# Kernel optimization log

Hardware: AMD Instinct MI355X
Metric: run time of the kernel (lower is better)

Reference implementation:

```python
import jax, jax.numpy as jnp
import numpy as np
import math

B, S, H, NH = 2, 2048, 2048, 16
HD = H // NH
LAYER_NUMBER = 5
NORM_FACTOR = math.sqrt(HD) * LAYER_NUMBER  # sqrt(head_dim) * coeff
BETA = 1.0 / LAYER_NUMBER
SCALE = float(LAYER_NUMBER)  # ScaledSoftmax scale = coeff
MASK_VALUE = -10000.0


def setup_inputs() -> dict:
    key = jax.random.key(0)
    ks = jax.random.split(key, 6)
    inv_sqrt_h = 1.0 / math.sqrt(H)
    return {
        "hidden_states": jax.random.normal(ks[0], (B, S, H), jnp.float32),
        "alibi": jax.random.normal(ks[1], (NH, 1, S), jnp.float32) * 0.1,
        "w_qkv": jax.random.normal(ks[2], (3 * H, H), jnp.float32) * inv_sqrt_h,
        "b_qkv": jax.random.normal(ks[3], (3 * H,), jnp.float32) * 0.02,
        "w_dense": jax.random.normal(ks[4], (H, H), jnp.float32) * inv_sqrt_h,
        "b_dense": jax.random.normal(ks[5], (H,), jnp.float32) * 0.02,
        "attention_mask": jnp.ones((B, S), jnp.int32),
    }


def reference(hidden_states, alibi, w_qkv, b_qkv, w_dense, b_dense, attention_mask):
    b, s, h = hidden_states.shape
    # QKV projection: [b, s, 3h] -> [b, s, nh, 3*hd] -> split
    mixed = hidden_states @ w_qkv.T + b_qkv
    mixed = mixed.reshape(b, s, NH, 3 * HD)
    q, k, v = jnp.split(mixed, 3, axis=-1)  # each [b, s, nh, hd]

    # Faithful Megatron-style memory reinterpretation (row-major reshape),
    # exactly matching torch's .contiguous().view(s, b*nh, hd).
    q2 = jnp.swapaxes(q.reshape(s, b * NH, HD), 0, 1)  # [b*nh, q_len, hd]
    k2 = jnp.swapaxes(k.reshape(s, b * NH, HD), 0, 1)  # [b*nh, k_len, hd]
    v2 = jnp.swapaxes(v.reshape(s, b * NH, HD), 0, 1)  # [b*nh, k_len, hd]

    # baddbmm: alibi*beta + (q @ k^T)/norm_factor
    alibi_b = jnp.tile(alibi, (b, 1, 1))[: b * NH, :, :s]  # [b*nh, 1, k_len]
    scores = alibi_b * BETA + jnp.einsum("bqd,bkd->bqk", q2, k2) * (1.0 / NORM_FACTOR)
    scores = scores.reshape(b, NH, s, s)

    # ScaledSoftmax: scale then fused causal+padding mask fill, then softmax
    scores = scores * SCALE
    pad_bool = (1 - attention_mask).astype(bool)  # True where padded
    causal = jnp.tril(jnp.ones((s, s), dtype=bool))
    bad = pad_bool[:, None, :, None] | (~causal)[None, None, :, :]  # [b,1,s,s]
    scores = jnp.where(bad, MASK_VALUE, scores)
    probs = jax.nn.softmax(scores, axis=-1)  # [b, nh, s, s]

    # context = probs @ V with the same faithful reshapes
    probs_r = probs.reshape(b * NH, s, s)
    context = jnp.einsum("bqk,bkd->bqd", probs_r, v2)  # [b*nh, q_len, hd]
    context = context.reshape(b, NH, s, HD)
    context = jnp.transpose(context, (2, 0, 1, 3)).reshape(s, b, h)  # [s, b, h]

    out = context @ w_dense.T + b_dense  # [s, b, h]
    return jnp.swapaxes(out, 0, 1)  # [b, s, h]
```

## Files before the change

### kernel.cpp

```cpp
#include <hip/hip_runtime.h>

typedef unsigned short u16;
typedef __bf16  bf16x8 __attribute__((ext_vector_type(8)));
typedef float   f32x4  __attribute__((ext_vector_type(4)));
typedef u16     u16x8  __attribute__((ext_vector_type(8)));
typedef u16     u16x4  __attribute__((ext_vector_type(4)));

#define QSCALE 0.12751744545f

__device__ __forceinline__ u16 f2b(float f) {
    unsigned u = __float_as_uint(f);
    unsigned r = u + 0x7FFFu + ((u >> 16) & 1u);
    return (u16)(r >> 16);
}
__device__ __forceinline__ float b2f(u16 b) {
    return __uint_as_float(((unsigned)b) << 16);
}
__device__ __forceinline__ void async16(const u16* g, u16* l) {
    __builtin_amdgcn_global_load_lds(
        (__attribute__((address_space(1))) void*)(u16*)g,
        (__attribute__((address_space(3))) void*)l, 16, 0, 0);
}

__global__ void cvt_f32_bf16(const float* __restrict__ in, u16* __restrict__ out, int n4) {
    int i = blockIdx.x * blockDim.x + threadIdx.x;
    if (i >= n4) return;
    float4 f = ((const float4*)in)[i];
    u16x4 o;
    o[0] = f2b(f.x); o[1] = f2b(f.y); o[2] = f2b(f.z); o[3] = f2b(f.w);
    *(u16x4*)(out + (size_t)i * 4) = o;
}

__global__ void cvt_wqkv(const float* __restrict__ in, u16* __restrict__ out, int n4) {
    int i = blockIdx.x * blockDim.x + threadIdx.x;
    if (i >= n4) return;
    int row = i >> 9;
    float s = ((row % 384) < 128) ? QSCALE : 1.0f;
    float4 f = ((const float4*)in)[i];
    u16x4 o;
    o[0] = f2b(f.x * s); o[1] = f2b(f.y * s); o[2] = f2b(f.z * s); o[3] = f2b(f.w * s);
    *(u16x4*)(out + (size_t)i * 4) = o;
}

__global__ __launch_bounds__(256) void gemm_bt(
    const u16* __restrict__ A, const u16* __restrict__ B,
    const float* __restrict__ bias, void* __restrict__ C,
    u16* __restrict__ qb, u16* __restrict__ kb, u16* __restrict__ vb,
    int M, int N, int K, int mode)
{
    __shared__ u16 smem[16384];
    u16* As = smem;
    u16* Bs = smem + 8192;

    int tid = threadIdx.x, wave = tid >> 6, lane = tid & 63;
    int lg = lane >> 4, lm = lane & 15;
    int wm = (wave & 1) * 64, wn = (wave >> 1) * 64;

    const u16* Ab = A + (size_t)(blockIdx.y * 128) * K;
    const u16* Bb = B + (size_t)(blockIdx.x * 128) * K;

    f32x4 acc[4][4];
    for (int i = 0; i < 4; i++)
        for (int j = 0; j < 4; j++)
            acc[i][j] = (f32x4){0.f, 0.f, 0.f, 0.f};

    int srow = (lane >> 2), skq = (lane & 3) * 8;

    for (int k0 = 0; k0 < K; k0 += 64) {
        __syncthreads();
        for (int cc = wave; cc < 16; cc += 4) {
            int p = cc >> 3, c = cc & 7;
            int row = c * 16 + srow;
            size_t off = (size_t)row * K + k0 + p * 32 + skq;
            async16(Ab + off, &As[p * 4096 + c * 512]);
            async16(Bb + off, &Bs[p * 4096 + c * 512]);
        }
        __syncthreads();

        for (int p = 0; p < 2; p++) {
            bf16x8 af[4], bf[4];
            for (int i = 0; i < 4; i++) af[i] = *(const bf16x8*)&As[p * 4096 + (wm + i * 16 + lm) * 32 + lg * 8];
            for (int j = 0; j < 4; j++) bf[j] = *(const bf16x8*)&Bs[p * 4096 + (wn + j * 16 + lm) * 32 + lg * 8];
            for (int i = 0; i < 4; i++)
                for (int j = 0; j < 4; j++)
                    acc[i][j] = __builtin_amdgcn_mfma_f32_16x16x32_bf16(af[i], bf[j], acc[i][j], 0, 0, 0);
        }
    }

    if (mode == 1) {
        for (int j = 0; j < 4; j++) {
            int col = blockIdx.x * 128 + wn + j * 16 + lm;
            float bv = bias[col];
            for (int i = 0; i < 4; i++) {
                int row0 = blockIdx.y * 128 + wm + i * 16 + lg * 4;
                for (int r = 0; r < 4; r++) {
                    int row = row0 + r;
                    int orow = ((row & 1) << 11) + (row >> 1);
                    ((float*)C)[(size_t)orow * N + col] = acc[i][j][r] + bv;
                }
            }
        }
        return;
    }

    int ct = blockIdx.x;
    int nh = ct / 3, part = ct - nh * 3;
    float bscale = (part == 0) ? QSCALE : 1.0f;
    int rbase = blockIdx.y * 128;
    int b = rbase >> 11;
    int s0 = rbase & 2047;

    if (part < 2) {
        u16* dst0 = part ? kb : qb;
        for (int j = 0; j < 4; j++) {
            int hd = wn + j * 16 + lm;
            float bv = bias[ct * 128 + hd] * bscale;
            for (int i = 0; i < 4; i++) {
                for (int r = 0; r < 4; r++) {
                    int rl = wm + i * 16 + lg * 4 + r;
                    int s = s0 + rl;
                    int bn = (s & 1) * 16 + nh;
                    int pos = (b << 10) + (s >> 1);
                    dst0[((size_t)(bn * 2048 + pos)) * 128 + hd] = f2b(acc[i][j][r] + bv);
                }
            }
        }
    } else {
        u16 (*arr)[64][128] = (u16(*)[64][128])smem;
        __syncthreads();
        for (int j = 0; j < 4; j++) {
            int hd = wn + j * 16 + lm;
            float bv = bias[ct * 128 + hd];
            for (int i = 0; i < 4; i++) {
                for (int r = 0; r < 4; r++) {
                    int rl = wm + i * 16 + lg * 4 + r;
                    arr[rl & 1][rl >> 1][hd] = f2b(acc[i][j][r] + bv);
                }
            }
        }
        __syncthreads();
        int hd = tid & 127, par = tid >> 7;
        int bn = par * 16 + nh;
        int pos0 = (b << 10) + (s0 >> 1);
        u16* dst = vb + ((size_t)(bn * 128 + hd)) * 2048 + pos0;
        for (int c = 0; c < 8; c++) {
            u16x8 w;
            for (int e = 0; e < 8; e++) w[e] = arr[par][c * 8 + e][hd];
            *(u16x8*)(dst + c * 8) = w;
        }
    }
}

__global__ __launch_bounds__(256) void attn(
    const u16* __restrict__ qb, const u16* __restrict__ kb,
    const u16* __restrict__ vb, const float* __restrict__ alibi,
    u16* __restrict__ ctx)
{
    __shared__ u16 Ks[64 * 136];
    __shared__ u16 Vt[128 * 88];
    __shared__ u16 Ps[4][16 * 72];

    int bn = blockIdx.y;
    int tid = threadIdx.x, wave = tid >> 6, lane = tid & 63;
    int lg = lane >> 4, lm = lane & 15;

    const float* al = alibi + (bn & 15) * 2048;

    int krow = tid >> 2, kq = (tid & 3) * 32;
    int vhd  = tid >> 1, vh2 = (tid & 1) * 32;
    const u16* ksrc0 = kb + (size_t)(bn * 2048 + krow) * 128 + kq;
    const u16* vsrc0 = vb + (size_t)(bn * 128 + vhd) * 2048 + vh2;

    u16* ps = &Ps[wave][0];
    bf16x8 ones;
    {
        u16x8 t;
        for (int j = 0; j < 8; j++) t[j] = 0x3F80;
        ones = *(bf16x8*)&t;
    }

    for (int pass = 0; pass < 2; pass++) {
        int qt = pass ? (31 - blockIdx.x) : blockIdx.x;
        int q0 = qt * 64;

        bf16x8 qf[4];
        {
            const u16* qp = qb + ((size_t)bn * 2048 + q0 + wave * 16 + lm) * 128 + lg * 8;
            for (int kc = 0; kc < 4; kc++) qf[kc] = *(const bf16x8*)(qp + kc * 32);
        }

        f32x4 o[9];
        for (int i = 0; i < 9; i++) o[i] = (f32x4){0.f, 0.f, 0.f, 0.f};

        u16x8 kreg[4], vreg[4];
        for (int i = 0; i < 4; i++) kreg[i] = *(const u16x8*)(ksrc0 + i * 8);
        for (int i = 0; i < 4; i++) vreg[i] = *(const u16x8*)(vsrc0 + i * 8);

        for (int kt = 0; kt <= qt; kt++) {
            int k0 = kt * 64;
            __syncthreads();
            {
                u16* d1 = &Ks[krow * 136 + kq];
                for (int i = 0; i < 4; i++) *(u16x8*)(d1 + i * 8) = kreg[i];
                u16* d2 = &Vt[vhd * 88 + vh2];
                for (int i = 0; i < 4; i++) *(u16x8*)(d2 + i * 8) = vreg[i];
            }
            __syncthreads();

            if (kt < qt) {
                const u16* s1 = ksrc0 + (size_t)(kt + 1) * 64 * 128;
                const u16* s2 = vsrc0 + (kt + 1) * 64;
                for (int i = 0; i < 4; i++) kreg[i] = *(const u16x8*)(s1 + i * 8);
                for (int i = 0; i < 4; i++) vreg[i] = *(const u16x8*)(s2 + i * 8);
            }

            f32x4 sc[4];
            for (int tc = 0; tc < 4; tc++) {
                const u16* kr = &Ks[(tc * 16 + lm) * 136 + lg * 8];
                f32x4 a = (f32x4){0.f, 0.f, 0.f, 0.f};
                for (int kc = 0; kc < 4; kc++)
                    a = __builtin_amdgcn_mfma_f32_16x16x32_bf16(qf[kc], *(const bf16x8*)(kr + kc * 32), a, 0, 0, 0);
                sc[tc] = a;
            }

            bool diag = (kt == qt);
            for (int tc = 0; tc < 4; tc++) {
                int kg = k0 + tc * 16 + lm;
                float av = (al[kg] - 8.0f) * 1.4426950408889634f;
                for (int r = 0; r < 4; r++) {
                    float v = sc[tc][r] + av;
                    if (diag && kg > q0 + wave * 16 + lg * 4 + r) v = -3e38f;
                    ps[(lg * 4 + r) * 72 + tc * 16 + lm] = f2b(__builtin_amdgcn_exp2f(v));
                }
            }

            for (int kc = 0; kc < 2; kc++) {
                bf16x8 pf = *(const bf16x8*)&ps[lm * 72 + kc * 32 + lg * 8];
                for (int i = 0; i < 8; i++) {
                    bf16x8 vf = *(const bf16x8*)&Vt[(i * 16 + lm) * 88 + kc * 32 + lg * 8];
                    o[i] = __builtin_amdgcn_mfma_f32_16x16x32_bf16(pf, vf, o[i], 0, 0, 0);
                }
                o[8] = __builtin_amdgcn_mfma_f32_16x16x32_bf16(pf, ones, o[8], 0, 0, 0);
            }
        }

        for (int r = 0; r < 4; r++) {
            float inv = 1.0f / o[8][r];
            int qg = q0 + wave * 16 + lg * 4 + r;
            int row = qg * 2 + (bn >> 4);
            u16* crow = ctx + (size_t)row * 2048 + (bn & 15) * 128 + lm;
            for (int i = 0; i < 8; i++)
                crow[i * 16] = f2b(o[i][r] * inv);
        }
    }
}

extern "C" void kernel_launch(void* const* d_in, const int* in_sizes, int n_in,
                              void* d_out, int out_size, void* d_ws, size_t ws_size,
                              hipStream_t stream)
{
    const float* hs    = (const float*)d_in[0];
    const float* alibi = (const float*)d_in[1];
    const float* wqkv  = (const float*)d_in[2];
    const float* bqkv  = (const float*)d_in[3];
    const float* wd    = (const float*)d_in[4];
    const float* bd    = (const float*)d_in[5];
    float* out = (float*)d_out;

    char* ws = (char*)d_ws;
    u16* wqkv_b = (u16*)(ws + 0);
    u16* hs_b   = (u16*)(ws + 25165824);
    u16* ctx    = (u16*)(ws + 41943040);
    u16* wd_b   = wqkv_b;
    u16* qb     = (u16*)(ws + 92274688);
    u16* kb     = (u16*)(ws + 109051904);
    u16* vb     = (u16*)(ws + 125829120);

    cvt_f32_bf16<<<8192,  256, 0, stream>>>(hs,   hs_b,   2097152);
    cvt_wqkv   <<<12288, 256, 0, stream>>>(wqkv, wqkv_b, 3145728);

    gemm_bt<<<dim3(48, 32), 256, 0, stream>>>(hs_b, wqkv_b, bqkv, nullptr,
                                              qb, kb, vb, 4096, 6144, 2048, 0);

    cvt_f32_bf16<<<4096, 256, 0, stream>>>(wd, wd_b, 1048576);

    attn<<<dim3(16, 32), 256, 0, stream>>>(qb, kb, vb, alibi, ctx);

    gemm_bt<<<dim3(16, 32), 256, 0, stream>>>(ctx, wd_b, bd, out,
                                              nullptr, nullptr, nullptr, 4096, 2048, 2048, 1);
}
```

Before: 396.6 us.

## Pipeline GEMM with triple-buffered async LDS ring and restructure attention tiles

The GEMM now uses a three-slot LDS ring filled by async global-to-LDS loads two K-steps ahead. It adds XOR-swizzled LDS addressing, split MFMA phases with s_setprio and explicit vmcnt waits instead of full syncthreads per K step. The attention kernel drops the two-pass 64-row scheme for one 128-row query tile per block. It double-buffers K/V via async loads into swizzled LDS and computes two 16-row fragments per wave so K/V fragments are reused. The aim is to hide global latency and cut LDS bank conflicts, at the cost of more LDS use and harder scheduling, and the query-tile pairing that balanced causal work across blocks is gone.

Measured after the change: 479.7 us. +21.0%, slower.

```diff
diff --git a/kernel.cpp b/kernel.cpp
--- a/kernel.cpp
+++ b/kernel.cpp
@@ -12,9 +12,6 @@
     unsigned u = __float_as_uint(f);
     unsigned r = u + 0x7FFFu + ((u >> 16) & 1u);
     return (u16)(r >> 16);
-}
-__device__ __forceinline__ float b2f(u16 b) {
-    return __uint_as_float(((unsigned)b) << 16);
 }
 __device__ __forceinline__ void async16(const u16* g, u16* l) {
     __builtin_amdgcn_global_load_lds(
@@ -42,49 +39,82 @@
     *(u16x4*)(out + (size_t)i * 4) = o;
 }
 
-__global__ __launch_bounds__(256) void gemm_bt(
+__global__ __launch_bounds__(256) void gemm_ring(
     const u16* __restrict__ A, const u16* __restrict__ B,
     const float* __restrict__ bias, void* __restrict__ C,
     u16* __restrict__ qb, u16* __restrict__ kb, u16* __restrict__ vb,
-    int M, int N, int K, int mode)
+    int mode)
 {
-    __shared__ u16 smem[16384];
-    u16* As = smem;
-    u16* Bs = smem + 8192;
-
-    int tid = threadIdx.x, wave = tid >> 6, lane = tid & 63;
-    int lg = lane >> 4, lm = lane & 15;
-    int wm = (wave & 1) * 64, wn = (wave >> 1) * 64;
+    constexpr int K  = 2048;
+    constexpr int NS = 64;
+    __shared__ u16 lds[24576];
+
+    const int tid = threadIdx.x, wave = tid >> 6, lane = tid & 63;
+    const int lg = lane >> 4, lm = lane & 15;
+    const int wm = (wave & 1) * 64, wn = (wave >> 1) * 64;
 
     const u16* Ab = A + (size_t)(blockIdx.y * 128) * K;
     const u16* Bb = B + (size_t)(blockIdx.x * 128) * K;
+
+    const int srow = lane >> 2;
+    const int scs  = ((lane & 3) ^ ((lane >> 3) & 3)) * 8;
+
+    auto stage_h = [&](int s_, int slot, int j0) {
+        size_t k0 = (size_t)s_ * 32;
+        for (int j = j0; j < j0 + 2; j++) {
+            int cc = wave + 4 * j;
+            const u16* src = (cc < 8) ? Ab : Bb;
+            int c8 = cc & 7;
+            async16(src + (size_t)(c8 * 16 + srow) * K + k0 + scs,
+                    &lds[slot * 8192 + (cc < 8 ? 0 : 4096) + c8 * 512]);
+        }
+    };
+
+    const int coff = (lg ^ ((lm >> 1) & 3)) * 8;
 
     f32x4 acc[4][4];
     for (int i = 0; i < 4; i++)
         for (int j = 0; j < 4; j++)
             acc[i][j] = (f32x4){0.f, 0.f, 0.f, 0.f};
 
-    int srow = (lane >> 2), skq = (lane & 3) * 8;
-
-    for (int k0 = 0; k0 < K; k0 += 64) {
-        __syncthreads();
-        for (int cc = wave; cc < 16; cc += 4) {
-            int p = cc >> 3, c = cc & 7;
-            int row = c * 16 + srow;
-            size_t off = (size_t)row * K + k0 + p * 32 + skq;
-            async16(Ab + off, &As[p * 4096 + c * 512]);
-            async16(Bb + off, &Bs[p * 4096 + c * 512]);
-        }
-        __syncthreads();
-
-        for (int p = 0; p < 2; p++) {
-            bf16x8 af[4], bf[4];
-            for (int i = 0; i < 4; i++) af[i] = *(const bf16x8*)&As[p * 4096 + (wm + i * 16 + lm) * 32 + lg * 8];
-            for (int j = 0; j < 4; j++) bf[j] = *(const bf16x8*)&Bs[p * 4096 + (wn + j * 16 + lm) * 32 + lg * 8];
-            for (int i = 0; i < 4; i++)
-                for (int j = 0; j < 4; j++)
-                    acc[i][j] = __builtin_amdgcn_mfma_f32_16x16x32_bf16(af[i], bf[j], acc[i][j], 0, 0, 0);
-        }
+    stage_h(0, 0, 0); stage_h(0, 0, 2);
+    stage_h(1, 1, 0); stage_h(1, 1, 2);
+    asm volatile("s_waitcnt vmcnt(4)" ::: "memory");
+    __builtin_amdgcn_s_barrier();
+
+    int slc = 0;
+    for (int s = 0; s < NS; s++) {
+        const u16* sa = &lds[slc * 8192];
+        const u16* sb = sa + 4096;
+        int st = slc + 2; if (st >= 3) st -= 3;
+
+        bf16x8 af[4], bf[4];
+        for (int i = 0; i < 4; i++) af[i] = *(const bf16x8*)&sa[(wm + i * 16 + lm) * 32 + coff];
+        for (int j = 0; j < 2; j++) bf[j] = *(const bf16x8*)&sb[(wn + j * 16 + lm) * 32 + coff];
+        if (s + 2 < NS) stage_h(s + 2, st, 0);
+        __builtin_amdgcn_s_barrier();
+        __builtin_amdgcn_s_setprio(1);
+        for (int i = 0; i < 4; i++)
+            for (int j = 0; j < 2; j++)
+                acc[i][j] = __builtin_amdgcn_mfma_f32_16x16x32_bf16(af[i], bf[j], acc[i][j], 0, 0, 0);
+        __builtin_amdgcn_s_setprio(0);
+        __builtin_amdgcn_s_barrier();
+
+        for (int j = 2; j < 4; j++) bf[j] = *(const bf16x8*)&sb[(wn + j * 16 + lm) * 32 + coff];
+        if (s + 2 < NS) stage_h(s + 2, st, 2);
+        __builtin_amdgcn_s_barrier();
+        __builtin_amdgcn_s_setprio(1);
+        for (int i = 0; i < 4; i++)
+            for (int j = 2; j < 4; j++)
+                acc[i][j] = __builtin_amdgcn_mfma_f32_16x16x32_bf16(af[i], bf[j], acc[i][j], 0, 0, 0);
+        __builtin_amdgcn_s_setprio(0);
+
+        if (s + 1 < NS) {
+            if (s + 2 < NS) asm volatile("s_waitcnt vmcnt(4)" ::: "memory");
+            else            asm volatile("s_waitcnt vmcnt(0)" ::: "memory");
+            __builtin_amdgcn_s_barrier();
+        }
+        slc++; if (slc == 3) slc = 0;
     }
 
     if (mode == 1) {
@@ -96,7 +126,7 @@
                 for (int r = 0; r < 4; r++) {
                     int row = row0 + r;
                     int orow = ((row & 1) << 11) + (row >> 1);
-                    ((float*)C)[(size_t)orow * N + col] = acc[i][j][r] + bv;
+                    ((float*)C)[(size_t)orow * 2048 + col] = acc[i][j][r] + bv;
                 }
             }
         }
@@ -126,7 +156,7 @@
             }
         }
     } else {
-        u16 (*arr)[64][128] = (u16(*)[64][128])smem;
+        u16 (*arr)[64][128] = (u16(*)[64][128])lds;
         __syncthreads();
         for (int j = 0; j < 4; j++) {
             int hd = wn + j * 16 + lm;
@@ -156,20 +186,40 @@
     const u16* __restrict__ vb, const float* __restrict__ alibi,
     u16* __restrict__ ctx)
 {
-    __shared__ u16 Ks[64 * 136];
-    __shared__ u16 Vt[128 * 88];
-    __shared__ u16 Ps[4][16 * 72];
-
-    int bn = blockIdx.y;
-    int tid = threadIdx.x, wave = tid >> 6, lane = tid & 63;
-    int lg = lane >> 4, lm = lane & 15;
+    __shared__ u16 Ks2[2][64 * 128];
+    __shared__ u16 Vt2[2][128 * 64];
+    __shared__ u16 Ps[4][32 * 64];
+
+    const int bn = blockIdx.y;
+    const int qt = blockIdx.x;
+    const int q0 = qt * 128;
+    const int ktmax = 2 * qt + 1;
+
+    const int tid = threadIdx.x, wave = tid >> 6, lane = tid & 63;
+    const int lg = lane >> 4, lm = lane & 15;
+    const int rxor = (lm & 7) * 8;
+    const int qrow0 = q0 + wave * 32;
 
     const float* al = alibi + (bn & 15) * 2048;
 
-    int krow = tid >> 2, kq = (tid & 3) * 32;
-    int vhd  = tid >> 1, vh2 = (tid & 1) * 32;
-    const u16* ksrc0 = kb + (size_t)(bn * 2048 + krow) * 128 + kq;
-    const u16* vsrc0 = vb + (size_t)(bn * 128 + vhd) * 2048 + vh2;
+    const int krl = lane >> 4;
+    const u16* Kbase = kb + ((size_t)bn * 2048 + 16 * wave + krl) * 128;
+    const int kco0 = ((lane & 15) ^ krl) * 8;
+    const int kco1 = ((lane & 15) ^ (4 + krl)) * 8;
+    const int vl = lane >> 3;
+    const u16* Vbase = vb + ((size_t)(bn * 128 + 32 * wave) + vl) * 2048
+                          + (((lane & 7) ^ vl) * 8);
+
+    auto stage = [&](int buf, int kt) {
+        size_t k0 = (size_t)kt * 64;
+        u16* kd = &Ks2[buf][16 * wave * 128];
+        for (int i = 0; i < 4; i++)
+            async16(Kbase + (k0 + 4 * i) * 128 + ((i & 1) ? kco1 : kco0),
+                    kd + 4 * i * 128);
+        u16* vd = &Vt2[buf][32 * wave * 64];
+        for (int i = 0; i < 4; i++)
+            async16(Vbase + (size_t)i * 16384 + k0, vd + 8 * i * 64);
+    };
 
     u16* ps = &Ps[wave][0];
     bf16x8 ones;
@@ -179,78 +229,87 @@
         ones = *(bf16x8*)&t;
     }
 
-    for (int pass = 0; pass < 2; pass++) {
-        int qt = pass ? (31 - blockIdx.x) : blockIdx.x;
-        int q0 = qt * 64;
-
-        bf16x8 qf[4];
-        {
-            const u16* qp = qb + ((size_t)bn * 2048 + q0 + wave * 16 + lm) * 128 + lg * 8;
-            for (int kc = 0; kc < 4; kc++) qf[kc] = *(const bf16x8*)(qp + kc * 32);
-        }
-
-        f32x4 o[9];
-        for (int i = 0; i < 9; i++) o[i] = (f32x4){0.f, 0.f, 0.f, 0.f};
-
-        u16x8 kreg[4], vreg[4];
-        for (int i = 0; i < 4; i++) kreg[i] = *(const u16x8*)(ksrc0 + i * 8);
-        for (int i = 0; i < 4; i++) vreg[i] = *(const u16x8*)(vsrc0 + i * 8);
-
-        for (int kt = 0; kt <= qt; kt++) {
-            int k0 = kt * 64;
-            __syncthreads();
-            {
-                u16* d1 = &Ks[krow * 136 + kq];
-                for (int i = 0; i < 4; i++) *(u16x8*)(d1 + i * 8) = kreg[i];
-                u16* d2 = &Vt[vhd * 88 + vh2];
-                for (int i = 0; i < 4; i++) *(u16x8*)(d2 + i * 8) = vreg[i];
-            }
-            __syncthreads();
-
-            if (kt < qt) {
-                const u16* s1 = ksrc0 + (size_t)(kt + 1) * 64 * 128;
-                const u16* s2 = vsrc0 + (kt + 1) * 64;
-                for (int i = 0; i < 4; i++) kreg[i] = *(const u16x8*)(s1 + i * 8);
-                for (int i = 0; i < 4; i++) vreg[i] = *(const u16x8*)(s2 + i * 8);
-            }
-
-            f32x4 sc[4];
+    bf16x8 qf[2][4];
+    for (int f = 0; f < 2; f++) {
+        const u16* qp = qb + ((size_t)bn * 2048 + qrow0 + f * 16 + lm) * 128 + lg * 8;
+        for (int kc = 0; kc < 4; kc++) qf[f][kc] = *(const bf16x8*)(qp + kc * 32);
+    }
+
+    f32x4 o[2][9];
+    for (int f = 0; f < 2; f++)
+        for (int i = 0; i < 9; i++) o[f][i] = (f32x4){0.f, 0.f, 0.f, 0.f};
+
+    stage(0, 0);
+
+    for (int kt = 0; kt <= ktmax; kt++) {
+        int buf = kt & 1;
+        if (kt < ktmax) {
+            stage(buf ^ 1, kt + 1);
+            asm volatile("s_waitcnt vmcnt(8)" ::: "memory");
+        } else {
+            asm volatile("s_waitcnt vmcnt(0)" ::: "memory");
+        }
+        __builtin_amdgcn_s_barrier();
+
+        int k0 = kt * 64;
+        bool act = (k0 <= qrow0 + 31);
+        if (act) {
+            const u16* KsB = &Ks2[buf][0];
+            const u16* VtB = &Vt2[buf][0];
+
+            f32x4 sc[2][4];
             for (int tc = 0; tc < 4; tc++) {
-                const u16* kr = &Ks[(tc * 16 + lm) * 136 + lg * 8];
-                f32x4 a = (f32x4){0.f, 0.f, 0.f, 0.f};
+                const u16* kr = &KsB[(tc * 16 + lm) * 128];
+                bf16x8 krf[4];
                 for (int kc = 0; kc < 4; kc++)
-                    a = __builtin_amdgcn_mfma_f32_16x16x32_bf16(qf[kc], *(const bf16x8*)(kr + kc * 32), a, 0, 0, 0);
-                sc[tc] = a;
-            }
-
-            bool diag = (kt == qt);
+                    krf[kc] = *(const bf16x8*)&kr[(kc * 32 + lg * 8) ^ rxor];
+                for (int f = 0; f < 2; f++) {
+                    f32x4 a = (f32x4){0.f, 0.f, 0.f, 0.f};
+                    for (int kc = 0; kc < 4; kc++)
+                        a = __builtin_amdgcn_mfma_f32_16x16x32_bf16(qf[f][kc], krf[kc], a, 0, 0, 0);
+                    sc[f][tc] = a;
+                }
+            }
+
+            bool dz = (kt >= 2 * qt);
             for (int tc = 0; tc < 4; tc++) {
                 int kg = k0 + tc * 16 + lm;
                 float av = (al[kg] - 8.0f) * 1.4426950408889634f;
-                for (int r = 0; r < 4; r++) {
-                    float v = sc[tc][r] + av;
-                    if (diag && kg > q0 + wave * 16 + lg * 4 + r) v = -3e38f;
-                    ps[(lg * 4 + r) * 72 + tc * 16 + lm] = f2b(__builtin_amdgcn_exp2f(v));
+                for (int f = 0; f < 2; f++) {
+                    for (int r = 0; r < 4; r++) {
+                        float v = sc[f][tc][r] + av;
+                        if (dz && kg > qrow0 + f * 16 + lg * 4 + r) v = -3e38f;
+                        int row = f * 16 + lg * 4 + r;
+                        ps[row * 64 + ((tc * 16 + lm) ^ ((row & 7) * 8))] =
+                            f2b(__builtin_amdgcn_exp2f(v));
+                    }
                 }
             }
 
             for (int kc = 0; kc < 2; kc++) {
-                bf16x8 pf = *(const bf16x8*)&ps[lm * 72 + kc * 32 + lg * 8];
+                bf16x8 pf[2];
+                for (int f = 0; f < 2; f++)
+                    pf[f] = *(const bf16x8*)&ps[(f * 16 + lm) * 64 + ((kc * 32 + lg * 8) ^ rxor)];
                 for (int i = 0; i < 8; i++) {
-                    bf16x8 vf = *(const bf16x8*)&Vt[(i * 16 + lm) * 88 + kc * 32 + lg * 8];
-                    o[i] = __builtin_amdgcn_mfma_f32_16x16x32_bf16(pf, vf, o[i], 0, 0, 0);
-                }
-                o[8] = __builtin_amdgcn_mfma_f32_16x16x32_bf16(pf, ones, o[8], 0, 0, 0);
-            }
-        }
-
+                    bf16x8 vf = *(const bf16x8*)&VtB[(i * 16 + lm) * 64 + ((kc * 32 + lg * 8) ^ rxor)];
+                    for (int f = 0; f < 2; f++)
+                        o[f][i] = __builtin_amdgcn_mfma_f32_16x16x32_bf16(pf[f], vf, o[f][i], 0, 0, 0);
+                }
+                for (int f = 0; f < 2; f++)
+                    o[f][8] = __builtin_amdgcn_mfma_f32_16x16x32_bf16(pf[f], ones, o[f][8], 0, 0, 0);
+            }
+        }
+        __builtin_amdgcn_s_barrier();
+    }
+
+    for (int f = 0; f < 2; f++) {
         for (int r = 0; r < 4; r++) {
-            float inv = 1.0f / o[8][r];
-            int qg = q0 + wave * 16 + lg * 4 + r;
+            float inv = 1.0f / o[f][8][r];
+            int qg = qrow0 + f * 16 + lg * 4 + r;
             int row = qg * 2 + (bn >> 4);
             u16* crow = ctx + (size_t)row * 2048 + (bn & 15) * 128 + lm;
             for (int i = 0; i < 8; i++)
-                crow[i * 16] = f2b(o[i][r] * inv);
+                crow[i * 16] = f2b(o[f][i][r] * inv);
         }
     }
 }
@@ -279,13 +338,13 @@
     cvt_f32_bf16<<<8192,  256, 0, stream>>>(hs,   hs_b,   2097152);
     cvt_wqkv   <<<12288, 256, 0, stream>>>(wqkv, wqkv_b, 3145728);
 
-    gemm_bt<<<dim3(48, 32), 256, 0, stream>>>(hs_b, wqkv_b, bqkv, nullptr,
-                                              qb, kb, vb, 4096, 6144, 2048, 0);
+    gemm_ring<<<dim3(48, 32), 256, 0, stream>>>(hs_b, wqkv_b, bqkv, nullptr,
+                                                qb, kb, vb, 0);
 
     cvt_f32_bf16<<<4096, 256, 0, stream>>>(wd, wd_b, 1048576);
 
     attn<<<dim3(16, 32), 256, 0, stream>>>(qb, kb, vb, alibi, ctx);
 
-    gemm_bt<<<dim3(16, 32), 256, 0, stream>>>(ctx, wd_b, bd, out,
-                                              nullptr, nullptr, nullptr, 4096, 2048, 2048, 1);
-}
+    gemm_ring<<<dim3(16, 32), 256, 0, stream>>>(ctx, wd_b, bd, out,
+                                                nullptr, nullptr, nullptr, 1);
+}
```
